# Performance work log

Hardware: AMD Instinct MI355X
Metric: run time of the kernel (lower is better)

## Reference

```python
import jax, jax.numpy as jnp
import numpy as np

B, M, T = 16, 256, 128
D, H, L, V = 512, 8, 4, 32000
BOS = 32000
HD = D // H
NEG = -1e9


def _ln(x, g, b, eps=1e-5):
    m = x.mean(-1, keepdims=True)
    v = ((x - m) ** 2).mean(-1, keepdims=True)
    return (x - m) / jnp.sqrt(v + eps) * g + b


def _split(t):  # [B,S,D] -> [B,H,S,HD]
    return t.reshape(t.shape[0], t.shape[1], H, HD).transpose(0, 2, 1, 3)


def _merge(t):  # [B,H,S,HD] -> [B,S,D]
    return t.transpose(0, 2, 1, 3).reshape(t.shape[0], t.shape[2], D)


def setup_inputs() -> dict:
    key = jax.random.key(0)
    ks = jax.random.split(key, 40)
    rn = lambda k, shape, s=0.02: jax.random.normal(k, shape, jnp.float32) * s
    inp = {
        'memory': jax.random.normal(ks[0], (B, M, D), jnp.float32),
        'targets': jax.random.randint(ks[1], (B, T), 0, V, jnp.int64),
        'tok_emb': rn(ks[2], (V + 1, D)),
        'pos_emb': rn(ks[3], (T + 1, D)),
        'sa_qkv_w': rn(ks[4], (L, D, 3 * D)), 'sa_qkv_b': jnp.zeros((L, 3 * D)),
        'sa_out_w': rn(ks[5], (L, D, D)), 'sa_out_b': jnp.zeros((L, D)),
        'ca_q_w': rn(ks[6], (L, D, D)), 'ca_q_b': jnp.zeros((L, D)),
        'ca_kv_w': rn(ks[7], (L, D, 2 * D)), 'ca_kv_b': jnp.zeros((L, 2 * D)),
        'ca_out_w': rn(ks[8], (L, D, D)), 'ca_out_b': jnp.zeros((L, D)),
        'ffn1_w': rn(ks[9], (L, D, 4 * D)), 'ffn1_b': jnp.zeros((L, 4 * D)),
        'ffn2_w': rn(ks[10], (L, 4 * D, D)), 'ffn2_b': jnp.zeros((L, D)),
        'ln1_g': jnp.ones((L, D)), 'ln1_b': jnp.zeros((L, D)),
        'ln2_g': jnp.ones((L, D)), 'ln2_b': jnp.zeros((L, D)),
        'ln3_g': jnp.ones((L, D)), 'ln3_b': jnp.zeros((L, D)),
        'normf_g': jnp.ones((D,)), 'normf_b': jnp.zeros((D,)),
        'out_w': rn(ks[11], (D, V)), 'out_b': jnp.zeros((V,)),
    }
    return inp


def reference(memory, targets, tok_emb, pos_emb, sa_qkv_w, sa_qkv_b, sa_out_w,
              sa_out_b, ca_q_w, ca_q_b, ca_kv_w, ca_kv_b, ca_out_w, ca_out_b,
              ffn1_w, ffn1_b, ffn2_w, ffn2_b, ln1_g, ln1_b, ln2_g, ln2_b,
              ln3_g, ln3_b, normf_g, normf_b, out_w, out_b):
    # teacher forcing: prepend BOS, drop last target token
    bos = jnp.full((memory.shape[0], 1), BOS, dtype=targets.dtype)
    inp = jnp.concatenate([bos, targets[:, :-1]], axis=1)  # [B,T]
    S = inp.shape[1]
    x = tok_emb[inp] + pos_emb[jnp.arange(S)][None]  # [B,T,D]
    causal = jnp.tril(jnp.ones((S, S), bool))
    scale = 1.0 / np.sqrt(HD)
    for l in range(L):
        # self-attention (pre-norm)
        h = _ln(x, ln1_g[l], ln1_b[l])
        q, k, v = jnp.split(h @ sa_qkv_w[l] + sa_qkv_b[l], 3, axis=-1)
        q, k, v = _split(q), _split(k), _split(v)
        s = jnp.einsum('bhqd,bhkd->bhqk', q, k) * scale
        a = jax.nn.softmax(jnp.where(causal, s, NEG), axis=-1)
        x = x + _merge(jnp.einsum('bhqk,bhkd->bhqd', a, v)) @ sa_out_w[l] + sa_out_b[l]
        # cross-attention to memory
        h = _ln(x, ln2_g[l], ln2_b[l])
        q = _split(h @ ca_q_w[l] + ca_q_b[l])
        k, v = jnp.split(memory @ ca_kv_w[l] + ca_kv_b[l], 2, axis=-1)
        k, v = _split(k), _split(v)
        s = jnp.einsum('bhqd,bhkd->bhqk', q, k) * scale
        a = jax.nn.softmax(s, axis=-1)
        x = x + _merge(jnp.einsum('bhqk,bhkd->bhqd', a, v)) @ ca_out_w[l] + ca_out_b[l]
        # FFN (gelu, exact erf form as torch 'gelu')
        h = _ln(x, ln3_g[l], ln3_b[l])
        x = x + jax.nn.gelu(h @ ffn1_w[l] + ffn1_b[l], approximate=False) @ ffn2_w[l] + ffn2_b[l]
    x = _ln(x, normf_g, normf_b)
    return x @ out_w + out_b  # [B,T,V]
```

## Files before the change

### kernel.cpp

```cpp
#include <hip/hip_runtime.h>
#include <hip/hip_bf16.h>
#include <math.h>

#define BB 16
#define TT 128
#define MM 256
#define DD 512
#define HH 8
#define LL 4
#define VV 32000
#define BOS_TOK 32000

typedef __attribute__((ext_vector_type(8))) short s8v;
typedef __attribute__((ext_vector_type(4))) float f4v;

__device__ __forceinline__ float bs2f(short u) {
    union { unsigned int i; float f; } c;
    c.i = ((unsigned int)(unsigned short)u) << 16;
    return c.f;
}
__device__ __forceinline__ short f2bs(float f) {
    union { float f; unsigned int u; } c;
    c.f = f;
    unsigned int r = (c.u + 0x7FFFu + ((c.u >> 16) & 1u)) >> 16;
    return (short)r;
}

__global__ __launch_bounds__(256) void cvt_k(const float* __restrict__ src,
                                             short* __restrict__ dst, int n4) {
    int i = (blockIdx.x * 256 + threadIdx.x);
    if (i < n4) {
        f4v v = *(const f4v*)&src[i * 4];
#pragma unroll
        for (int j = 0; j < 4; j++) dst[i * 4 + j] = f2bs(v[j]);
    }
}

__global__ __launch_bounds__(256) void wt_k(const float* __restrict__ src,
                                            short* __restrict__ dst, int K, int N) {
    __shared__ short t[64][65];
    int k0 = blockIdx.x * 64, n0 = blockIdx.y * 64;
    size_t zo = (size_t)blockIdx.z * K * N;
    int tid = threadIdx.x;
    int kr = tid >> 2;
    int nc = (tid & 3) * 16;
    const float* sp = src + zo + (size_t)(k0 + kr) * N + n0 + nc;
#pragma unroll
    for (int c = 0; c < 4; c++) {
        f4v v = *(const f4v*)(sp + c * 4);
#pragma unroll
        for (int j = 0; j < 4; j++) t[kr][nc + c * 4 + j] = f2bs(v[j]);
    }
    __syncthreads();
    int nr = tid >> 2;
    int kc = (tid & 3) * 16;
    short* dp = dst + zo + (size_t)(n0 + nr) * K + k0 + kc;
#pragma unroll
    for (int c = 0; c < 2; c++) {
        s8v v;
#pragma unroll
        for (int j = 0; j < 8; j++) v[j] = t[kc + c * 8 + j][nr];
        *(s8v*)(dp + c * 8) = v;
    }
}

__global__ __launch_bounds__(256) void embed_k(const int* __restrict__ tgt,
                                               const float* __restrict__ tok,
                                               const float* __restrict__ pos,
                                               float* __restrict__ X) {
    int row = blockIdx.x;
    int t = row & (TT - 1);
    int b = row >> 7;
    int idx = (t == 0) ? BOS_TOK : tgt[b * TT + t - 1];
    const float* te = tok + (size_t)idx * DD;
    const float* pe = pos + (size_t)t * DD;
    float* xr = X + (size_t)row * DD;
    for (int d = threadIdx.x; d < DD; d += 256)
        xr[d] = te[d] + pe[d];
}

__global__ __launch_bounds__(256) void ln_k(const float* __restrict__ X,
                                            const float* __restrict__ g,
                                            const float* __restrict__ bta,
                                            short* __restrict__ H) {
    int row = blockIdx.x;
    int tid = threadIdx.x;
    const float* xr = X + (size_t)row * DD;
    float v0 = xr[tid], v1 = xr[tid + 256];
    float s = v0 + v1, ss = v0 * v0 + v1 * v1;
    for (int o = 32; o; o >>= 1) {
        s += __shfl_xor(s, o, 64);
        ss += __shfl_xor(ss, o, 64);
    }
    __shared__ float r0[4], r1[4];
    int wave = tid >> 6, lane = tid & 63;
    if (lane == 0) { r0[wave] = s; r1[wave] = ss; }
    __syncthreads();
    s = r0[0] + r0[1] + r0[2] + r0[3];
    ss = r1[0] + r1[1] + r1[2] + r1[3];
    float mean = s * (1.0f / DD);
    float var = ss * (1.0f / DD) - mean * mean;
    float rstd = rsqrtf(var + 1e-5f);
    short* hr = H + (size_t)row * DD;
    hr[tid] = f2bs((v0 - mean) * rstd * g[tid] + bta[tid]);
    hr[tid + 256] = f2bs((v1 - mean) * rstd * g[tid + 256] + bta[tid + 256]);
}

template <int EPI, int BM, int BN>
__global__ __launch_bounds__(256) void gemm_k(const short* __restrict__ A,
                                              const short* __restrict__ Bt,
                                              const float* __restrict__ bias,
                                              short* __restrict__ C,
                                              float* __restrict__ X, int M, int N, int K) {
    constexpr int MI = BM / 32;
    constexpr int NJ = BN / 32;
    __shared__ short Al[BM * 34];
    __shared__ short Bl[BN * 34];
    int tid = threadIdx.x, lane = tid & 63, wave = tid >> 6;
    int wm = wave >> 1, wn = wave & 1;
    int quad = lane >> 4, l16 = lane & 15;

    int nwg = gridDim.x * gridDim.y;
    int orig = blockIdx.y * gridDim.x + blockIdx.x;
    int q = nwg >> 3, r = nwg & 7;
    int xcd = orig & 7, pos = orig >> 3;
    int wg = (xcd < r ? xcd * (q + 1) : r * (q + 1) + (xcd - r) * q) + pos;
    int mt = wg % gridDim.x, nt = wg / gridDim.x;
    int m0 = mt * BM, n0 = nt * BN;

    f4v acc[MI][NJ];
#pragma unroll
    for (int i = 0; i < MI; i++)
#pragma unroll
        for (int j = 0; j < NJ; j++) acc[i][j] = (f4v){0.f, 0.f, 0.f, 0.f};

    constexpr int TPRA = 256 / BM;
    constexpr int CA = 32 / TPRA;
    int arow = tid / TPRA, acol = (tid % TPRA) * CA;
    constexpr int TPRB = 256 / BN;
    constexpr int CB = 32 / TPRB;
    int brow = tid / TPRB, bcol = (tid % TPRB) * CB;

    for (int k0 = 0; k0 < K; k0 += 32) {
#pragma unroll
        for (int c = 0; c < CA / 8; c++)
            *(s8v*)&Al[arow * 34 + acol + c * 8] =
                *(const s8v*)&A[(size_t)(m0 + arow) * K + k0 + acol + c * 8];
#pragma unroll
        for (int c = 0; c < CB / 8; c++)
            *(s8v*)&Bl[brow * 34 + bcol + c * 8] =
                *(const s8v*)&Bt[(size_t)(n0 + brow) * K + k0 + bcol + c * 8];
        __syncthreads();
        s8v af[MI], bf[NJ];
#pragma unroll
        for (int i = 0; i < MI; i++)
            af[i] = *(const s8v*)&Al[(wm * (BM / 2) + 16 * i + l16) * 34 + quad * 8];
#pragma unroll
        for (int j = 0; j < NJ; j++)
            bf[j] = *(const s8v*)&Bl[(wn * (BN / 2) + 16 * j + l16) * 34 + quad * 8];
#pragma unroll
        for (int i = 0; i < MI; i++)
#pragma unroll
            for (int j = 0; j < NJ; j++)
                acc[i][j] = __builtin_amdgcn_mfma_f32_16x16x32_bf16(af[i], bf[j], acc[i][j], 0, 0, 0);
        __syncthreads();
    }
#pragma unroll
    for (int i = 0; i < MI; i++) {
#pragma unroll
        for (int j = 0; j < NJ; j++) {
            int gc = n0 + wn * (BN / 2) + 16 * j + l16;
            float bz = bias[gc];
#pragma unroll
            for (int r2 = 0; r2 < 4; r2++) {
                int gr = m0 + wm * (BM / 2) + 16 * i + quad * 4 + r2;
                float v = acc[i][j][r2] + bz;
                if (EPI == 1) v = 0.5f * v * (1.0f + erff(v * 0.70710678118f));
                if (EPI == 2) {
                    size_t o = (size_t)gr * N + gc;
                    X[o] = X[o] + v;
                } else if (EPI == 3) {
                    X[(size_t)gr * N + gc] = v;
                } else {
                    C[(size_t)gr * N + gc] = f2bs(v);
                }
            }
        }
    }
}

template <int EPI>
__global__ __launch_bounds__(256) void gemm_w32_k(const short* __restrict__ A,
                                                  const float* __restrict__ W,
                                                  const float* __restrict__ bias,
                                                  short* __restrict__ C,
                                                  float* __restrict__ X, int M, int N, int K) {
    __shared__ short Al[64 * 32];
    __shared__ short Bl[32 * 66];
    int tid = threadIdx.x, lane = tid & 63, wave = tid >> 6;
    int wm = wave >> 1, wn = wave & 1;
    int quad = lane >> 4, l16 = lane & 15;
    int m0 = blockIdx.y * 64, n0 = blockIdx.x * 64;
    f4v acc[2][2];
#pragma unroll
    for (int i = 0; i < 2; i++)
#pragma unroll
        for (int j = 0; j < 2; j++) acc[i][j] = (f4v){0.f, 0.f, 0.f, 0.f};
    int arow = tid >> 2, acol = (tid & 3) * 8;
    int brow = tid >> 3, bcol = (tid & 7) * 8;
    for (int k0 = 0; k0 < K; k0 += 32) {
        *(s8v*)&Al[arow * 32 + acol] = *(const s8v*)&A[(size_t)(m0 + arow) * K + k0 + acol];
        const float* wp = &W[(size_t)(k0 + brow) * N + n0 + bcol];
        f4v wa = *(const f4v*)wp;
        f4v wb = *(const f4v*)(wp + 4);
#pragma unroll
        for (int j = 0; j < 4; j++) {
            Bl[brow * 66 + bcol + j] = f2bs(wa[j]);
            Bl[brow * 66 + bcol + 4 + j] = f2bs(wb[j]);
        }
        __syncthreads();
        s8v af[2], bf[2];
#pragma unroll
        for (int i = 0; i < 2; i++)
            af[i] = *(const s8v*)&Al[(32 * wm + 16 * i + l16) * 32 + quad * 8];
#pragma unroll
        for (int j = 0; j < 2; j++) {
            s8v t;
#pragma unroll
            for (int u = 0; u < 8; u++)
                t[u] = Bl[(quad * 8 + u) * 66 + 32 * wn + 16 * j + l16];
            bf[j] = t;
        }
#pragma unroll
        for (int i = 0; i < 2; i++)
#pragma unroll
            for (int j = 0; j < 2; j++)
                acc[i][j] = __builtin_amdgcn_mfma_f32_16x16x32_bf16(af[i], bf[j], acc[i][j], 0, 0, 0);
        __syncthreads();
    }
#pragma unroll
    for (int i = 0; i < 2; i++) {
#pragma unroll
        for (int j = 0; j < 2; j++) {
            int gc = n0 + 32 * wn + 16 * j + l16;
            float bz = bias[gc];
#pragma unroll
            for (int r = 0; r < 4; r++) {
                int gr = m0 + 32 * wm + 16 * i + quad * 4 + r;
                float v = acc[i][j][r] + bz;
                if (EPI == 1) v = 0.5f * v * (1.0f + erff(v * 0.70710678118f));
                if (EPI == 2) {
                    size_t o = (size_t)gr * N + gc;
                    X[o] = X[o] + v;
                } else if (EPI == 3) {
                    X[(size_t)gr * N + gc] = v;
                } else {
                    C[(size_t)gr * N + gc] = f2bs(v);
                }
            }
        }
    }
}

__global__ __launch_bounds__(256) void sattn_k(const short* __restrict__ qkv,
                                               short* __restrict__ attn) {
    int grp = blockIdx.x;
    int bh = blockIdx.y;
    int b = bh >> 3, h = bh & 7;
    __shared__ short Kl[128 * 66];
    __shared__ short Vl[128 * 66];
    __shared__ short Ql[32 * 66];
    __shared__ float pl[4][128];
    int tid = threadIdx.x, lane = tid & 63, wave = tid >> 6;
    size_t basek = ((size_t)b * TT) * 1536 + 512 + h * 64;
    size_t basev = basek + 512;
    for (int idx = tid; idx < 128 * 64; idx += 256) {
        int j = idx >> 6, d = idx & 63;
        Kl[j * 66 + d] = qkv[basek + (size_t)j * 1536 + d];
        Vl[j * 66 + d] = qkv[basev + (size_t)j * 1536 + d];
    }
    size_t baseq = ((size_t)b * TT + grp * 32) * 1536 + h * 64;
    for (int idx = tid; idx < 32 * 64; idx += 256) {
        int r = idx >> 6, d = idx & 63;
        Ql[r * 66 + d] = qkv[baseq + (size_t)r * 1536 + d];
    }
    __syncthreads();
    for (int i = 0; i < 8; i++) {
        int rl = wave * 8 + i, rg = grp * 32 + rl;
        float s0 = 0.f, s1 = 0.f;
        const short* qrow = &Ql[rl * 66];
        for (int d = 0; d < 64; d++) {
            float qd = bs2f(qrow[d]);
            s0 += qd * bs2f(Kl[lane * 66 + d]);
            s1 += qd * bs2f(Kl[(lane + 64) * 66 + d]);
        }
        s0 = (lane <= rg) ? s0 * 0.125f : -1e30f;
        s1 = (lane + 64 <= rg) ? s1 * 0.125f : -1e30f;
        float m = fmaxf(s0, s1);
        for (int o = 32; o; o >>= 1) m = fmaxf(m, __shfl_xor(m, o, 64));
        float e0 = expf(s0 - m), e1 = expf(s1 - m);
        float sm = e0 + e1;
        for (int o = 32; o; o >>= 1) sm += __shfl_xor(sm, o, 64);
        float inv = 1.0f / sm;
        pl[wave][lane] = e0 * inv;
        pl[wave][lane + 64] = e1 * inv;
        float oa = 0.f;
        for (int j = 0; j < 128; j++) oa += pl[wave][j] * bs2f(Vl[j * 66 + lane]);
        attn[((size_t)b * TT + rg) * DD + h * 64 + lane] = f2bs(oa);
    }
}

__global__ __launch_bounds__(256) void cattn_k(const short* __restrict__ qb,
                                               const short* __restrict__ kvb,
                                               short* __restrict__ attn) {
    int grp = blockIdx.x, bh = blockIdx.y;
    int b = bh >> 3, h = bh & 7;
    __shared__ short Kl[128 * 66];
    __shared__ short Vl[128 * 66];
    __shared__ short Ql[32 * 66];
    __shared__ float pl[4][128];
    int tid = threadIdx.x, lane = tid & 63, wave = tid >> 6;
    float om[8], osum[8], oacc[8];
#pragma unroll
    for (int i = 0; i < 8; i++) { om[i] = -1e30f; osum[i] = 0.f; oacc[i] = 0.f; }

    size_t baseq = ((size_t)b * TT + grp * 32) * DD + h * 64;
    for (int idx = tid; idx < 32 * 64; idx += 256) {
        int r = idx >> 6, d = idx & 63;
        Ql[r * 66 + d] = qb[baseq + (size_t)r * DD + d];
    }
    for (int half = 0; half < 2; half++) {
        __syncthreads();
        size_t basek = ((size_t)b * MM + half * 128) * 1024 + h * 64;
        size_t basev = basek + 512;
        for (int idx = tid; idx < 128 * 64; idx += 256) {
            int j = idx >> 6, d = idx & 63;
            Kl[j * 66 + d] = kvb[basek + (size_t)j * 1024 + d];
            Vl[j * 66 + d] = kvb[basev + (size_t)j * 1024 + d];
        }
        __syncthreads();
        for (int i = 0; i < 8; i++) {
            int rl = wave * 8 + i;
            float s0 = 0.f, s1 = 0.f;
            const short* qrow = &Ql[rl * 66];
            for (int d = 0; d < 64; d++) {
                float qd = bs2f(qrow[d]);
                s0 += qd * bs2f(Kl[lane * 66 + d]);
                s1 += qd * bs2f(Kl[(lane + 64) * 66 + d]);
            }
            s0 *= 0.125f;
            s1 *= 0.125f;
            float m = fmaxf(s0, s1);
            for (int o = 32; o; o >>= 1) m = fmaxf(m, __shfl_xor(m, o, 64));
            float mnew = fmaxf(om[i], m);
            float e0 = expf(s0 - mnew), e1 = expf(s1 - mnew);
            float ps = e0 + e1;
            for (int o = 32; o; o >>= 1) ps += __shfl_xor(ps, o, 64);
            float corr = expf(om[i] - mnew);
            osum[i] = osum[i] * corr + ps;
            oacc[i] = oacc[i] * corr;
            om[i] = mnew;
            pl[wave][lane] = e0;
            pl[wave][lane + 64] = e1;
            float oa = 0.f;
            for (int j = 0; j < 128; j++) oa += pl[wave][j] * bs2f(Vl[j * 66 + lane]);
            oacc[i] += oa;
        }
    }
#pragma unroll
    for (int i = 0; i < 8; i++) {
        int rg = grp * 32 + wave * 8 + i;
        attn[((size_t)b * TT + rg) * DD + h * 64 + lane] = f2bs(oacc[i] / osum[i]);
    }
}

extern "C" void kernel_launch(void* const* d_in, const int* in_sizes, int n_in, void* d_out,
                              int out_size, void* d_ws, size_t ws_size, hipStream_t stream) {
    (void)in_sizes; (void)n_in; (void)out_size;
    typedef const float* fp;
    fp memory = (fp)d_in[0];
    const int* targets = (const int*)d_in[1];
    fp tok = (fp)d_in[2];
    fp pos = (fp)d_in[3];
    fp saqkv_w = (fp)d_in[4], saqkv_b = (fp)d_in[5];
    fp saout_w = (fp)d_in[6], saout_b = (fp)d_in[7];
    fp caq_w = (fp)d_in[8], caq_b = (fp)d_in[9];
    fp cakv_w = (fp)d_in[10], cakv_b = (fp)d_in[11];
    fp caout_w = (fp)d_in[12], caout_b = (fp)d_in[13];
    fp f1w = (fp)d_in[14], f1b = (fp)d_in[15];
    fp f2w = (fp)d_in[16], f2bb = (fp)d_in[17];
    fp ln1g = (fp)d_in[18], ln1b = (fp)d_in[19];
    fp ln2g = (fp)d_in[20], ln2b = (fp)d_in[21];
    fp ln3g = (fp)d_in[22], ln3b = (fp)d_in[23];
    fp lnfg = (fp)d_in[24], lnfb = (fp)d_in[25];
    fp outw = (fp)d_in[26], outb = (fp)d_in[27];
    float* out = (float*)d_out;

    char* ws = (char*)d_ws;
    float* X = (float*)ws;
    short* Hb = (short*)(ws + (4u << 20));
    short* ATT = (short*)(ws + (6u << 20));
    short* MEMB = (short*)(ws + (8u << 20));
    short* QKV = (short*)(ws + (12u << 20));
    short* Qb = (short*)(ws + (12u << 20));
    short* KVb = (short*)(ws + (14u << 20));
    short* F1 = (short*)(ws + (12u << 20));

    size_t wo = (size_t)22u << 20;
    short* WTqkv = (short*)(ws + wo);
    short* WTso  = (short*)(ws + wo + 6291456u);
    short* WTcq  = (short*)(ws + wo + 8388608u);
    short* WTckv = (short*)(ws + wo + 10485760u);
    short* WTco  = (short*)(ws + wo + 14680064u);
    short* WTf1  = (short*)(ws + wo + 16777216u);
    short* WTf2  = (short*)(ws + wo + 25165824u);
    short* WTout = (short*)(ws + wo + 33554432u);
    const size_t WS_NEED = wo + 33554432u + 32768000u;

    const int R = BB * TT;
    cvt_k<<<(BB * MM * DD / 4 + 255) / 256, 256, 0, stream>>>(memory, MEMB, BB * MM * DD / 4);
    embed_k<<<R, 256, 0, stream>>>(targets, tok, pos, X);

    if (ws_size >= WS_NEED) {
        wt_k<<<dim3(8, 24, LL), 256, 0, stream>>>(saqkv_w, WTqkv, DD, 1536);
        wt_k<<<dim3(8, 8, LL), 256, 0, stream>>>(saout_w, WTso, DD, DD);
        wt_k<<<dim3(8, 8, LL), 256, 0, stream>>>(caq_w, WTcq, DD, DD);
        wt_k<<<dim3(8, 16, LL), 256, 0, stream>>>(cakv_w, WTckv, DD, 1024);
        wt_k<<<dim3(8, 8, LL), 256, 0, stream>>>(caout_w, WTco, DD, DD);
        wt_k<<<dim3(8, 32, LL), 256, 0, stream>>>(f1w, WTf1, DD, 2048);
        wt_k<<<dim3(32, 8, LL), 256, 0, stream>>>(f2w, WTf2, 2048, DD);
        wt_k<<<dim3(8, 500, 1), 256, 0, stream>>>(outw, WTout, DD, VV);

        for (int l = 0; l < LL; l++) {
            ln_k<<<R, 256, 0, stream>>>(X, ln1g + l * DD, ln1b + l * DD, Hb);
            gemm_k<0, 128, 64><<<dim3(R / 128, 1536 / 64), 256, 0, stream>>>(
                Hb, WTqkv + (size_t)l * 1536 * DD, saqkv_b + l * 1536, QKV, nullptr, R, 1536, DD);
            sattn_k<<<dim3(4, BB * HH), 256, 0, stream>>>(QKV, ATT);
            gemm_k<2, 64, 64><<<dim3(R / 64, DD / 64), 256, 0, stream>>>(
                ATT, WTso + (size_t)l * DD * DD, saout_b + l * DD, nullptr, X, R, DD, DD);
            ln_k<<<R, 256, 0, stream>>>(X, ln2g + l * DD, ln2b + l * DD, Hb);
            gemm_k<0, 64, 64><<<dim3(R / 64, DD / 64), 256, 0, stream>>>(
                Hb, WTcq + (size_t)l * DD * DD, caq_b + l * DD, Qb, nullptr, R, DD, DD);
            gemm_k<0, 128, 128><<<dim3((BB * MM) / 128, 1024 / 128), 256, 0, stream>>>(
                MEMB, WTckv + (size_t)l * 1024 * DD, cakv_b + l * 1024, KVb, nullptr, BB * MM, 1024, DD);
            cattn_k<<<dim3(4, BB * HH), 256, 0, stream>>>(Qb, KVb, ATT);
            gemm_k<2, 64, 64><<<dim3(R / 64, DD / 64), 256, 0, stream>>>(
                ATT, WTco + (size_t)l * DD * DD, caout_b + l * DD, nullptr, X, R, DD, DD);
            ln_k<<<R, 256, 0, stream>>>(X, ln3g + l * DD, ln3b + l * DD, Hb);
            gemm_k<1, 128, 128><<<dim3(R / 128, 2048 / 128), 256, 0, stream>>>(
                Hb, WTf1 + (size_t)l * 2048 * DD, f1b + l * 2048, F1, nullptr, R, 2048, DD);
            gemm_k<2, 64, 64><<<dim3(R / 64, DD / 64), 256, 0, stream>>>(
                F1, WTf2 + (size_t)l * DD * 2048, f2bb + l * DD, nullptr, X, R, DD, 2048);
        }
        ln_k<<<R, 256, 0, stream>>>(X, lnfg, lnfb, Hb);
        gemm_k<3, 128, 128><<<dim3(R / 128, VV / 128), 256, 0, stream>>>(
            Hb, WTout, outb, nullptr, out, R, VV, DD);
    } else {
        for (int l = 0; l < LL; l++) {
            ln_k<<<R, 256, 0, stream>>>(X, ln1g + l * DD, ln1b + l * DD, Hb);
            gemm_w32_k<0><<<dim3(1536 / 64, R / 64), 256, 0, stream>>>(
                Hb, saqkv_w + (size_t)l * DD * 1536, saqkv_b + l * 1536, QKV, nullptr, R, 1536, DD);
            sattn_k<<<dim3(4, BB * HH), 256, 0, stream>>>(QKV, ATT);
            gemm_w32_k<2><<<dim3(DD / 64, R / 64), 256, 0, stream>>>(
                ATT, saout_w + (size_t)l * DD * DD, saout_b + l * DD, nullptr, X, R, DD, DD);
            ln_k<<<R, 256, 0, stream>>>(X, ln2g + l * DD, ln2b + l * DD, Hb);
            gemm_w32_k<0><<<dim3(DD / 64, R / 64), 256, 0, stream>>>(
                Hb, caq_w + (size_t)l * DD * DD, caq_b + l * DD, Qb, nullptr, R, DD, DD);
            gemm_w32_k<0><<<dim3(1024 / 64, (BB * MM) / 64), 256, 0, stream>>>(
                MEMB, cakv_w + (size_t)l * DD * 1024, cakv_b + l * 1024, KVb, nullptr, BB * MM, 1024, DD);
            cattn_k<<<dim3(4, BB * HH), 256, 0, stream>>>(Qb, KVb, ATT);
            gemm_w32_k<2><<<dim3(DD / 64, R / 64), 256, 0, stream>>>(
                ATT, caout_w + (size_t)l * DD * DD, caout_b + l * DD, nullptr, X, R, DD, DD);
            ln_k<<<R, 256, 0, stream>>>(X, ln3g + l * DD, ln3b + l * DD, Hb);
            gemm_w32_k<1><<<dim3(2048 / 64, R / 64), 256, 0, stream>>>(
                Hb, f1w + (size_t)l * DD * 2048, f1b + l * 2048, F1, nullptr, R, 2048, DD);
            gemm_w32_k<2><<<dim3(DD / 64, R / 64), 256, 0, stream>>>(
                F1, f2w + (size_t)l * 2048 * DD, f2bb + l * DD, nullptr, X, R, DD, 2048);
        }
        ln_k<<<R, 256, 0, stream>>>(X, lnfg, lnfb, Hb);
        gemm_w32_k<3><<<dim3(VV / 64, R / 64), 256, 0, stream>>>(Hb, outw, outb, nullptr, out, R, VV, DD);
    }
}
```

Measured before the change: 1.438 ms.

## Rewrite self and cross attention kernels to use bf16 MFMA instructions

Replaces the scalar per-lane dot-product attention kernels with MFMA 16x16x32 bf16 versions. Each block now handles 64 query rows; QK^T and PV both run as matrix instructions, with V transposed into LDS and probabilities staged as bf16. Self-attention splits into two causal halves of 64 and 128 keys, so the first half skips the masked keys. Cross-attention loads all 256 memory keys at once and does a single softmax instead of an online one. The cost is more LDS per block and rounding the probabilities to bf16.

```diff
diff --git a/kernel.cpp b/kernel.cpp
--- a/kernel.cpp
+++ b/kernel.cpp
@@ -262,116 +262,223 @@
     }
 }
 
-__global__ __launch_bounds__(256) void sattn_k(const short* __restrict__ qkv,
-                                               short* __restrict__ attn) {
-    int grp = blockIdx.x;
-    int bh = blockIdx.y;
-    int b = bh >> 3, h = bh & 7;
-    __shared__ short Kl[128 * 66];
-    __shared__ short Vl[128 * 66];
-    __shared__ short Ql[32 * 66];
-    __shared__ float pl[4][128];
+template <int NK>
+__device__ __forceinline__ void sattn_body(const short* __restrict__ qkv,
+                                           short* __restrict__ attn,
+                                           short* Ql, short* Kl, short* Vt, short* Pl,
+                                           int b, int h) {
+    constexpr int QBASE = NK - 64;
+    constexpr int NJ = NK / 16;
+    constexpr int QS = 72, KS = 72, VS = NK + 8, PS = NK + 8;
     int tid = threadIdx.x, lane = tid & 63, wave = tid >> 6;
+    int quad = lane >> 4, l16 = lane & 15;
+    size_t baseq = ((size_t)b * TT + QBASE) * 1536 + h * 64;
     size_t basek = ((size_t)b * TT) * 1536 + 512 + h * 64;
     size_t basev = basek + 512;
-    for (int idx = tid; idx < 128 * 64; idx += 256) {
-        int j = idx >> 6, d = idx & 63;
-        Kl[j * 66 + d] = qkv[basek + (size_t)j * 1536 + d];
-        Vl[j * 66 + d] = qkv[basev + (size_t)j * 1536 + d];
-    }
-    size_t baseq = ((size_t)b * TT + grp * 32) * 1536 + h * 64;
-    for (int idx = tid; idx < 32 * 64; idx += 256) {
-        int r = idx >> 6, d = idx & 63;
-        Ql[r * 66 + d] = qkv[baseq + (size_t)r * 1536 + d];
+    {
+        int row = tid >> 2, c = (tid & 3) * 16;
+        *(s8v*)&Ql[row * QS + c] = *(const s8v*)&qkv[baseq + (size_t)row * 1536 + c];
+        *(s8v*)&Ql[row * QS + c + 8] = *(const s8v*)&qkv[baseq + (size_t)row * 1536 + c + 8];
+    }
+    for (int idx = tid; idx < NK * 4; idx += 256) {
+        int row = idx >> 2, c = (idx & 3) * 16;
+        *(s8v*)&Kl[row * KS + c] = *(const s8v*)&qkv[basek + (size_t)row * 1536 + c];
+        *(s8v*)&Kl[row * KS + c + 8] = *(const s8v*)&qkv[basek + (size_t)row * 1536 + c + 8];
+    }
+    for (int idx = tid; idx < NK * 4; idx += 256) {
+        int key = idx >> 2, c = (idx & 3) * 16;
+        s8v v0 = *(const s8v*)&qkv[basev + (size_t)key * 1536 + c];
+        s8v v1 = *(const s8v*)&qkv[basev + (size_t)key * 1536 + c + 8];
+#pragma unroll
+        for (int u = 0; u < 8; u++) {
+            Vt[(c + u) * VS + key] = v0[u];
+            Vt[(c + 8 + u) * VS + key] = v1[u];
+        }
     }
     __syncthreads();
-    for (int i = 0; i < 8; i++) {
-        int rl = wave * 8 + i, rg = grp * 32 + rl;
-        float s0 = 0.f, s1 = 0.f;
-        const short* qrow = &Ql[rl * 66];
-        for (int d = 0; d < 64; d++) {
-            float qd = bs2f(qrow[d]);
-            s0 += qd * bs2f(Kl[lane * 66 + d]);
-            s1 += qd * bs2f(Kl[(lane + 64) * 66 + d]);
-        }
-        s0 = (lane <= rg) ? s0 * 0.125f : -1e30f;
-        s1 = (lane + 64 <= rg) ? s1 * 0.125f : -1e30f;
-        float m = fmaxf(s0, s1);
-        for (int o = 32; o; o >>= 1) m = fmaxf(m, __shfl_xor(m, o, 64));
-        float e0 = expf(s0 - m), e1 = expf(s1 - m);
-        float sm = e0 + e1;
-        for (int o = 32; o; o >>= 1) sm += __shfl_xor(sm, o, 64);
-        float inv = 1.0f / sm;
-        pl[wave][lane] = e0 * inv;
-        pl[wave][lane + 64] = e1 * inv;
-        float oa = 0.f;
-        for (int j = 0; j < 128; j++) oa += pl[wave][j] * bs2f(Vl[j * 66 + lane]);
-        attn[((size_t)b * TT + rg) * DD + h * 64 + lane] = f2bs(oa);
-    }
-}
-
-__global__ __launch_bounds__(256) void cattn_k(const short* __restrict__ qb,
+    s8v af[2];
+#pragma unroll
+    for (int kc = 0; kc < 2; kc++)
+        af[kc] = *(const s8v*)&Ql[(wave * 16 + l16) * QS + kc * 32 + quad * 8];
+    f4v s[NJ];
+#pragma unroll
+    for (int j = 0; j < NJ; j++) s[j] = (f4v){0.f, 0.f, 0.f, 0.f};
+#pragma unroll
+    for (int j = 0; j < NJ; j++) {
+#pragma unroll
+        for (int kc = 0; kc < 2; kc++) {
+            s8v bf = *(const s8v*)&Kl[(j * 16 + l16) * KS + kc * 32 + quad * 8];
+            s[j] = __builtin_amdgcn_mfma_f32_16x16x32_bf16(af[kc], bf, s[j], 0, 0, 0);
+        }
+    }
+    float sum[4];
+#pragma unroll
+    for (int r = 0; r < 4; r++) {
+        int grow = QBASE + wave * 16 + quad * 4 + r;
+        float m = -1e30f;
+#pragma unroll
+        for (int j = 0; j < NJ; j++) {
+            int col = j * 16 + l16;
+            float v = (col <= grow) ? s[j][r] * 0.125f : -1e30f;
+            s[j][r] = v;
+            m = fmaxf(m, v);
+        }
+        for (int o = 8; o; o >>= 1) m = fmaxf(m, __shfl_xor(m, o, 64));
+        float sm = 0.f;
+#pragma unroll
+        for (int j = 0; j < NJ; j++) {
+            float e = expf(s[j][r] - m);
+            s[j][r] = e;
+            sm += e;
+        }
+        for (int o = 8; o; o >>= 1) sm += __shfl_xor(sm, o, 64);
+        sum[r] = sm;
+    }
+#pragma unroll
+    for (int j = 0; j < NJ; j++)
+#pragma unroll
+        for (int r = 0; r < 4; r++)
+            Pl[(wave * 16 + quad * 4 + r) * PS + j * 16 + l16] = f2bs(s[j][r]);
+    __syncthreads();
+    f4v o[4];
+#pragma unroll
+    for (int j2 = 0; j2 < 4; j2++) o[j2] = (f4v){0.f, 0.f, 0.f, 0.f};
+#pragma unroll
+    for (int kc = 0; kc < NK / 32; kc++) {
+        s8v pa = *(const s8v*)&Pl[(wave * 16 + l16) * PS + kc * 32 + quad * 8];
+#pragma unroll
+        for (int j2 = 0; j2 < 4; j2++) {
+            s8v bv = *(const s8v*)&Vt[(j2 * 16 + l16) * VS + kc * 32 + quad * 8];
+            o[j2] = __builtin_amdgcn_mfma_f32_16x16x32_bf16(pa, bv, o[j2], 0, 0, 0);
+        }
+    }
+    float inv[4];
+#pragma unroll
+    for (int r = 0; r < 4; r++) inv[r] = 1.0f / sum[r];
+#pragma unroll
+    for (int j2 = 0; j2 < 4; j2++)
+#pragma unroll
+        for (int r = 0; r < 4; r++) {
+            int grow = QBASE + wave * 16 + quad * 4 + r;
+            attn[((size_t)b * TT + grow) * DD + h * 64 + j2 * 16 + l16] = f2bs(o[j2][r] * inv[r]);
+        }
+}
+
+__global__ __launch_bounds__(256) void sattn_m(const short* __restrict__ qkv,
+                                               short* __restrict__ attn) {
+    __shared__ short Ql[64 * 72];
+    __shared__ short Kl[128 * 72];
+    __shared__ short Vt[64 * 136];
+    __shared__ short Pl[64 * 136];
+    int bh = blockIdx.x;
+    int b = bh >> 3, h = bh & 7;
+    if (blockIdx.y == 0)
+        sattn_body<64>(qkv, attn, Ql, Kl, Vt, Pl, b, h);
+    else
+        sattn_body<128>(qkv, attn, Ql, Kl, Vt, Pl, b, h);
+}
+
+__global__ __launch_bounds__(256) void cattn_m(const short* __restrict__ qb,
                                                const short* __restrict__ kvb,
                                                short* __restrict__ attn) {
-    int grp = blockIdx.x, bh = blockIdx.y;
+    constexpr int NJ = 16;
+    constexpr int QS = 72, KS = 72, VS = 264, PS = 264;
+    __shared__ short Ql[64 * QS];
+    __shared__ short Kl[256 * KS];
+    __shared__ short Vt[64 * VS];
+    __shared__ short Pl[64 * PS];
+    int bh = blockIdx.x, grp = blockIdx.y;
     int b = bh >> 3, h = bh & 7;
-    __shared__ short Kl[128 * 66];
-    __shared__ short Vl[128 * 66];
-    __shared__ short Ql[32 * 66];
-    __shared__ float pl[4][128];
     int tid = threadIdx.x, lane = tid & 63, wave = tid >> 6;
-    float om[8], osum[8], oacc[8];
-#pragma unroll
-    for (int i = 0; i < 8; i++) { om[i] = -1e30f; osum[i] = 0.f; oacc[i] = 0.f; }
-
-    size_t baseq = ((size_t)b * TT + grp * 32) * DD + h * 64;
-    for (int idx = tid; idx < 32 * 64; idx += 256) {
-        int r = idx >> 6, d = idx & 63;
-        Ql[r * 66 + d] = qb[baseq + (size_t)r * DD + d];
-    }
-    for (int half = 0; half < 2; half++) {
-        __syncthreads();
-        size_t basek = ((size_t)b * MM + half * 128) * 1024 + h * 64;
-        size_t basev = basek + 512;
-        for (int idx = tid; idx < 128 * 64; idx += 256) {
-            int j = idx >> 6, d = idx & 63;
-            Kl[j * 66 + d] = kvb[basek + (size_t)j * 1024 + d];
-            Vl[j * 66 + d] = kvb[basev + (size_t)j * 1024 + d];
-        }
-        __syncthreads();
-        for (int i = 0; i < 8; i++) {
-            int rl = wave * 8 + i;
-            float s0 = 0.f, s1 = 0.f;
-            const short* qrow = &Ql[rl * 66];
-            for (int d = 0; d < 64; d++) {
-                float qd = bs2f(qrow[d]);
-                s0 += qd * bs2f(Kl[lane * 66 + d]);
-                s1 += qd * bs2f(Kl[(lane + 64) * 66 + d]);
-            }
-            s0 *= 0.125f;
-            s1 *= 0.125f;
-            float m = fmaxf(s0, s1);
-            for (int o = 32; o; o >>= 1) m = fmaxf(m, __shfl_xor(m, o, 64));
-            float mnew = fmaxf(om[i], m);
-            float e0 = expf(s0 - mnew), e1 = expf(s1 - mnew);
-            float ps = e0 + e1;
-            for (int o = 32; o; o >>= 1) ps += __shfl_xor(ps, o, 64);
-            float corr = expf(om[i] - mnew);
-            osum[i] = osum[i] * corr + ps;
-            oacc[i] = oacc[i] * corr;
-            om[i] = mnew;
-            pl[wave][lane] = e0;
-            pl[wave][lane + 64] = e1;
-            float oa = 0.f;
-            for (int j = 0; j < 128; j++) oa += pl[wave][j] * bs2f(Vl[j * 66 + lane]);
-            oacc[i] += oa;
-        }
-    }
-#pragma unroll
-    for (int i = 0; i < 8; i++) {
-        int rg = grp * 32 + wave * 8 + i;
-        attn[((size_t)b * TT + rg) * DD + h * 64 + lane] = f2bs(oacc[i] / osum[i]);
-    }
+    int quad = lane >> 4, l16 = lane & 15;
+    size_t baseq = ((size_t)b * TT + grp * 64) * DD + h * 64;
+    size_t basek = ((size_t)b * MM) * 1024 + h * 64;
+    size_t basev = basek + 512;
+    {
+        int row = tid >> 2, c = (tid & 3) * 16;
+        *(s8v*)&Ql[row * QS + c] = *(const s8v*)&qb[baseq + (size_t)row * DD + c];
+        *(s8v*)&Ql[row * QS + c + 8] = *(const s8v*)&qb[baseq + (size_t)row * DD + c + 8];
+    }
+    for (int idx = tid; idx < 256 * 4; idx += 256) {
+        int row = idx >> 2, c = (idx & 3) * 16;
+        *(s8v*)&Kl[row * KS + c] = *(const s8v*)&kvb[basek + (size_t)row * 1024 + c];
+        *(s8v*)&Kl[row * KS + c + 8] = *(const s8v*)&kvb[basek + (size_t)row * 1024 + c + 8];
+    }
+    for (int idx = tid; idx < 256 * 4; idx += 256) {
+        int key = idx >> 2, c = (idx & 3) * 16;
+        s8v v0 = *(const s8v*)&kvb[basev + (size_t)key * 1024 + c];
+        s8v v1 = *(const s8v*)&kvb[basev + (size_t)key * 1024 + c + 8];
+#pragma unroll
+        for (int u = 0; u < 8; u++) {
+            Vt[(c + u) * VS + key] = v0[u];
+            Vt[(c + 8 + u) * VS + key] = v1[u];
+        }
+    }
+    __syncthreads();
+    s8v af[2];
+#pragma unroll
+    for (int kc = 0; kc < 2; kc++)
+        af[kc] = *(const s8v*)&Ql[(wave * 16 + l16) * QS + kc * 32 + quad * 8];
+    f4v s[NJ];
+#pragma unroll
+    for (int j = 0; j < NJ; j++) s[j] = (f4v){0.f, 0.f, 0.f, 0.f};
+#pragma unroll
+    for (int j = 0; j < NJ; j++) {
+#pragma unroll
+        for (int kc = 0; kc < 2; kc++) {
+            s8v bf = *(const s8v*)&Kl[(j * 16 + l16) * KS + kc * 32 + quad * 8];
+            s[j] = __builtin_amdgcn_mfma_f32_16x16x32_bf16(af[kc], bf, s[j], 0, 0, 0);
+        }
+    }
+    float sum[4];
+#pragma unroll
+    for (int r = 0; r < 4; r++) {
+        float m = -1e30f;
+#pragma unroll
+        for (int j = 0; j < NJ; j++) {
+            float v = s[j][r] * 0.125f;
+            s[j][r] = v;
+            m = fmaxf(m, v);
+        }
+        for (int o = 8; o; o >>= 1) m = fmaxf(m, __shfl_xor(m, o, 64));
+        float sm = 0.f;
+#pragma unroll
+        for (int j = 0; j < NJ; j++) {
+            float e = expf(s[j][r] - m);
+            s[j][r] = e;
+            sm += e;
+        }
+        for (int o = 8; o; o >>= 1) sm += __shfl_xor(sm, o, 64);
+        sum[r] = sm;
+    }
+#pragma unroll
+    for (int j = 0; j < NJ; j++)
+#pragma unroll
+        for (int r = 0; r < 4; r++)
+            Pl[(wave * 16 + quad * 4 + r) * PS + j * 16 + l16] = f2bs(s[j][r]);
+    __syncthreads();
+    f4v o[4];
+#pragma unroll
+    for (int j2 = 0; j2 < 4; j2++) o[j2] = (f4v){0.f, 0.f, 0.f, 0.f};
+#pragma unroll
+    for (int kc = 0; kc < 8; kc++) {
+        s8v pa = *(const s8v*)&Pl[(wave * 16 + l16) * PS + kc * 32 + quad * 8];
+#pragma unroll
+        for (int j2 = 0; j2 < 4; j2++) {
+            s8v bv = *(const s8v*)&Vt[(j2 * 16 + l16) * VS + kc * 32 + quad * 8];
+            o[j2] = __builtin_amdgcn_mfma_f32_16x16x32_bf16(pa, bv, o[j2], 0, 0, 0);
+        }
+    }
+    float inv[4];
+#pragma unroll
+    for (int r = 0; r < 4; r++) inv[r] = 1.0f / sum[r];
+#pragma unroll
+    for (int j2 = 0; j2 < 4; j2++)
+#pragma unroll
+        for (int r = 0; r < 4; r++) {
+            int grow = grp * 64 + wave * 16 + quad * 4 + r;
+            attn[((size_t)b * TT + grow) * DD + h * 64 + j2 * 16 + l16] = f2bs(o[j2][r] * inv[r]);
+        }
 }
 
 extern "C" void kernel_launch(void* const* d_in, const int* in_sizes, int n_in, void* d_out,
@@ -435,7 +542,7 @@
             ln_k<<<R, 256, 0, stream>>>(X, ln1g + l * DD, ln1b + l * DD, Hb);
             gemm_k<0, 128, 64><<<dim3(R / 128, 1536 / 64), 256, 0, stream>>>(
                 Hb, WTqkv + (size_t)l * 1536 * DD, saqkv_b + l * 1536, QKV, nullptr, R, 1536, DD);
-            sattn_k<<<dim3(4, BB * HH), 256, 0, stream>>>(QKV, ATT);
+            sattn_m<<<dim3(BB * HH, 2), 256, 0, stream>>>(QKV, ATT);
             gemm_k<2, 64, 64><<<dim3(R / 64, DD / 64), 256, 0, stream>>>(
                 ATT, WTso + (size_t)l * DD * DD, saout_b + l * DD, nullptr, X, R, DD, DD);
             ln_k<<<R, 256, 0, stream>>>(X, ln2g + l * DD, ln2b + l * DD, Hb);
@@ -443,7 +550,7 @@
                 Hb, WTcq + (size_t)l * DD * DD, caq_b + l * DD, Qb, nullptr, R, DD, DD);
             gemm_k<0, 128, 128><<<dim3((BB * MM) / 128, 1024 / 128), 256, 0, stream>>>(
                 MEMB, WTckv + (size_t)l * 1024 * DD, cakv_b + l * 1024, KVb, nullptr, BB * MM, 1024, DD);
-            cattn_k<<<dim3(4, BB * HH), 256, 0, stream>>>(Qb, KVb, ATT);
+            cattn_m<<<dim3(BB * HH, 2), 256, 0, stream>>>(Qb, KVb, ATT);
             gemm_k<2, 64, 64><<<dim3(R / 64, DD / 64), 256, 0, stream>>>(
                 ATT, WTco + (size_t)l * DD * DD, caout_b + l * DD, nullptr, X, R, DD, DD);
             ln_k<<<R, 256, 0, stream>>>(X, ln3g + l * DD, ln3b + l * DD, Hb);
@@ -460,7 +567,7 @@
             ln_k<<<R, 256, 0, stream>>>(X, ln1g + l * DD, ln1b + l * DD, Hb);
             gemm_w32_k<0><<<dim3(1536 / 64, R / 64), 256, 0, stream>>>(
                 Hb, saqkv_w + (size_t)l * DD * 1536, saqkv_b + l * 1536, QKV, nullptr, R, 1536, DD);
-            sattn_k<<<dim3(4, BB * HH), 256, 0, stream>>>(QKV, ATT);
+            sattn_m<<<dim3(BB * HH, 2), 256, 0, stream>>>(QKV, ATT);
             gemm_w32_k<2><<<dim3(DD / 64, R / 64), 256, 0, stream>>>(
                 ATT, saout_w + (size_t)l * DD * DD, saout_b + l * DD, nullptr, X, R, DD, DD);
             ln_k<<<R, 256, 0, stream>>>(X, ln2g + l * DD, ln2b + l * DD, Hb);
@@ -468,7 +575,7 @@
                 Hb, caq_w + (size_t)l * DD * DD, caq_b + l * DD, Qb, nullptr, R, DD, DD);
             gemm_w32_k<0><<<dim3(1024 / 64, (BB * MM) / 64), 256, 0, stream>>>(
                 MEMB, cakv_w + (size_t)l * DD * 1024, cakv_b + l * 1024, KVb, nullptr, BB * MM, 1024, DD);
-            cattn_k<<<dim3(4, BB * HH), 256, 0, stream>>>(Qb, KVb, ATT);
+            cattn_m<<<dim3(BB * HH, 2), 256, 0, stream>>>(Qb, KVb, ATT);
             gemm_w32_k<2><<<dim3(DD / 64, R / 64), 256, 0, stream>>>(
                 ATT, caout_w + (size_t)l * DD * DD, caout_b + l * DD, nullptr, X, R, DD, DD);
             ln_k<<<R, 256, 0, stream>>>(X, ln3g + l * DD, ln3b + l * DD, Hb);
```

Result: faster. 1.176 ms (-18.2%).
